# Optimization experiments

Measured on AMD Instinct MI355X. Metric: run time of the kernel, lower is better.

The kernel has to match this reference:

```python
import jax, jax.numpy as jnp
import numpy as np

B, T, C, H = 1, 1024, 2048, 32
N = C // H  # head_dim = 64
EPS_GN = 0.00064


def setup_inputs() -> dict:
    key = jax.random.key(0)
    ks = jax.random.split(key, 40)
    f32 = jnp.float32

    def rn(k, shape, s):
        return jax.random.normal(k, shape, f32) * s

    layer_idx, n_layer = 12, 24
    r01 = layer_idx / (n_layer - 1)
    r1a0 = 1.0 - layer_idx / n_layer
    ddd = (jnp.arange(C, dtype=f32) / C).reshape(1, 1, C)
    decay_speed = -7.0 + 5.0 * (jnp.arange(C, dtype=f32) / (C - 1)) ** (0.85 + r01 ** 0.5)

    inp = dict(
        hidden_states=jax.random.normal(ks[0], (B, T, C), f32),
        Wq=rn(ks[1], (C, C), 0.02), Wk=rn(ks[2], (C, C), 0.02),
        Wv=rn(ks[3], (C, C), 0.02), Wo=rn(ks[4], (C, C), 0.02),
        time_maa_x=1.0 - ddd ** (0.6 * r1a0 ** 0.9),
        time_maa_rg=rn(ks[5], (1, 1, C), 0.01),
        time_maa_wa=rn(ks[6], (1, 1, C), 0.01),
        time_maa_k=rn(ks[7], (1, 1, C), 0.01),
        time_maa_v=rn(ks[8], (1, 1, C), 0.01),
        time_maa_w1=rn(ks[9], (C, 4 * 32), 0.01),
        time_maa_w2=rn(ks[10], (4, 32, C), 0.01),
        time_decay=decay_speed.reshape(1, 1, C) + 0.5,
        time_decay_w1=rn(ks[11], (C, 64), 0.01),
        time_decay_w2=rn(ks[12], (64, C), 0.01),
        time_aaaaa=rn(ks[13], (1, 1, C), 0.01),
        time_aaa_w1=rn(ks[14], (C, 16), 0.01),
        time_aaa_w2=rn(ks[15], (16, C), 0.01),
        time_kkk_w1=rn(ks[16], (C, 16), 0.01),
        time_kkk_w2=rn(ks[17], (16, C), 0.01),
        gate_w1=rn(ks[18], (C, 128), 0.01),
        gate_w2=rn(ks[19], (128, C), 0.01),
        time_misc_a=rn(ks[20], (1, 1, C), 0.01),
        ma_w1=rn(ks[21], (C, 16), 0.01),
        ma_w2=rn(ks[22], (16, C), 0.01),
        time_misc_k=rn(ks[23], (1, 1, C), 0.01),
        mk_w1=rn(ks[24], (C, 16), 0.01),
        mk_w2=rn(ks[25], (16, C), 0.01),
        time_faaaa=rn(ks[26], (1, 1, H, N), 0.01),
        ln_w=1.0 + rn(ks[27], (C,), 0.01),
        ln_b=rn(ks[28], (C,), 0.01),
    )
    return inp


def _wkv7(r, w, k, v, a, b):
    """RWKV7 matrix-state recurrence. Inputs [B,T,C]; per head state [N,N].
    state_t = state * exp(w_t) (per key-col) + (state @ a_t) b_t^T + v_t k_t^T;
    out_t = state_t @ r_t."""
    hs = lambda x: x.reshape(B, T, H, N)
    r, k, v, a, b = map(hs, (r, k, v, a, b))
    dec = jnp.exp(hs(w))  # w <= -0.5, decay in (0,1)

    def step(state, inp):
        r_t, d_t, k_t, v_t, a_t, b_t = inp  # each [B,H,N]
        sa = jnp.einsum('bhij,bhj->bhi', state, a_t)
        state = (state * d_t[:, :, None, :]
                 + sa[..., None] * b_t[:, :, None, :]
                 + v_t[..., None] * k_t[:, :, None, :])
        out = jnp.einsum('bhij,bhj->bhi', state, r_t)
        return state, out

    xs = tuple(jnp.moveaxis(t, 1, 0) for t in (r, dec, k, v, a, b))  # [T,B,H,N]
    state0 = jnp.zeros((B, H, N, N), r.dtype)
    _, out = jax.lax.scan(step, state0, xs)
    return jnp.moveaxis(out, 0, 1).reshape(B, T, C)


def _group_norm(x, w, b):
    xg = x.reshape(B, T, H, N)
    mu = xg.mean(-1, keepdims=True)
    var = xg.var(-1, keepdims=True)
    xn = (xg - mu) * jax.lax.rsqrt(var + EPS_GN)
    return xn.reshape(B, T, C) * w + b


def reference(hidden_states, Wq, Wk, Wv, Wo, time_maa_x, time_maa_rg, time_maa_wa,
              time_maa_k, time_maa_v, time_maa_w1, time_maa_w2, time_decay,
              time_decay_w1, time_decay_w2, time_aaaaa, time_aaa_w1, time_aaa_w2,
              time_kkk_w1, time_kkk_w2, gate_w1, gate_w2, time_misc_a, ma_w1, ma_w2,
              time_misc_k, mk_w1, mk_w2, time_faaaa, ln_w, ln_b):
    x = hidden_states  # T already multiple of 16, so no padding branch
    dxprev = jnp.pad(x, ((0, 0), (1, 0), (0, 0)))[:, :-1] - x  # token shift
    xxx = x + dxprev * time_maa_x
    mix = jnp.tanh(xxx @ time_maa_w1).reshape(B, T, 4, 32)
    mix = jnp.einsum('btfd,fdc->fbtc', mix, time_maa_w2)  # [4,B,T,C]
    mrg, mwa, mk_mix, mv = mix[0], mix[1], mix[2], mix[3]
    xrg = x + dxprev * (time_maa_rg + mrg)
    xwa = x + dxprev * (time_maa_wa + mwa)
    xk = x + dxprev * (time_maa_k + mk_mix)
    xv = x + dxprev * (time_maa_v + mv)

    r = xrg @ Wq
    w = -jax.nn.softplus(-(time_decay + jnp.tanh(xwa @ time_decay_w1) @ time_decay_w2)) - 0.5
    k = xk @ Wk
    v = xv @ Wv
    g = jnp.tanh(xrg @ gate_w1) @ gate_w2

    kk = k + jnp.tanh(xk @ time_kkk_w1) @ time_kkk_w2
    kkh = kk.reshape(B, T, H, N)
    kk = (kkh / jnp.maximum(jnp.linalg.norm(kkh, axis=-1, keepdims=True), 1e-12)).reshape(B, T, C)

    a = jax.nn.sigmoid(time_aaaaa + (xwa @ time_aaa_w1) @ time_aaa_w2)
    ma = jax.nn.sigmoid(time_misc_a + (xwa @ ma_w1) @ ma_w2)
    k = k * ma + k * a * (1.0 - ma)
    mk_g = jax.nn.sigmoid(time_misc_k + (xk @ mk_w1) @ mk_w2)
    k = k * jnp.exp(jnp.minimum(w * mk_g, 0.0))

    y = _wkv7(r, w, k, v, -kk, kk * a)
    y = _group_norm(y, ln_w, ln_b)
    rh, kh, vh = (t.reshape(B, T, H, N) for t in (r, k, v))
    y = y + ((rh * kh * time_faaaa).sum(-1, keepdims=True) * vh).reshape(B, T, C)
    return (y * g) @ Wo
```

## Files before the change

kernel.cpp:

```cpp
#include <hip/hip_runtime.h>


#define T_ 1024
#define C_ 2048
#define H_ 32
#define N_ 64

using half8  = __attribute__((ext_vector_type(8))) _Float16;
using half4  = __attribute__((ext_vector_type(4))) _Float16;
using floatx4 = __attribute__((ext_vector_type(4))) float;

#define DPP_ADD(v, ctrl) \
    ((v) + __int_as_float(__builtin_amdgcn_update_dpp( \
        0, __float_as_int(v), (ctrl), 0xf, 0xf, true)))
#define REDUCE16(v) do { \
    v = DPP_ADD(v, 0xB1); v = DPP_ADD(v, 0x4E); \
    v = DPP_ADD(v, 0x141); v = DPP_ADD(v, 0x140); } while (0)

__device__ __forceinline__ void async_cp16(const void* g, void* l) {
    __builtin_amdgcn_global_load_lds(
        (const __attribute__((address_space(1))) void*)g,
        (__attribute__((address_space(3))) void*)l, 16, 0, 0);
}

__global__ __launch_bounds__(256) void k_tr(
    const float* __restrict__ W0, const float* __restrict__ W1,
    const float* __restrict__ W2, const float* __restrict__ W3,
    _Float16* __restrict__ D0, _Float16* __restrict__ D1,
    _Float16* __restrict__ D2, _Float16* __restrict__ D3)
{
    const int z = blockIdx.z;
    const float* S = (z == 0) ? W0 : (z == 1) ? W1 : (z == 2) ? W2 : W3;
    _Float16* D = (z == 0) ? D0 : (z == 1) ? D1 : (z == 2) ? D2 : D3;
    const int nb = blockIdx.x * 64, kb = blockIdx.y * 64;
    __shared__ __align__(16) float tile[64][65];
    const int tr = threadIdx.x >> 4, tc4 = (threadIdx.x & 15) * 4;
#pragma unroll
    for (int p = 0; p < 4; ++p) {
        int row = p * 16 + tr;
        float4 v = *(const float4*)&S[(size_t)(kb + row) * C_ + nb + tc4];
        tile[row][tc4 + 0] = v.x; tile[row][tc4 + 1] = v.y;
        tile[row][tc4 + 2] = v.z; tile[row][tc4 + 3] = v.w;
    }
    __syncthreads();
#pragma unroll
    for (int p = 0; p < 4; ++p) {
        int n = p * 16 + tr;
        half4 u;
        u[0] = (_Float16)tile[tc4 + 0][n];
        u[1] = (_Float16)tile[tc4 + 1][n];
        u[2] = (_Float16)tile[tc4 + 2][n];
        u[3] = (_Float16)tile[tc4 + 3][n];
        *(half4*)&D[(size_t)(nb + n) * C_ + kb + tc4] = u;
    }
}

__global__ __launch_bounds__(256) void k_trW(
    const float* __restrict__ maa_w1, const float* __restrict__ gate_w1,
    const float* __restrict__ decay_w1, const float* __restrict__ aaa_w1,
    const float* __restrict__ ma_w1, const float* __restrict__ kkk_w1,
    const float* __restrict__ mk_w1,
    _Float16* __restrict__ WTm, _Float16* __restrict__ WTl)
{
    const int z = blockIdx.z;
    const int k = blockIdx.x * 256 + threadIdx.x;
    const int n = blockIdx.y;
    if (z == 0 && n >= 128) return;
    const float* src; int stride, col;
    _Float16* dst;
    if (z == 0) { src = maa_w1; stride = 128; col = n; dst = WTm; }
    else {
        dst = WTl;
        if (n < 128)      { src = gate_w1;  stride = 128; col = n; }
        else if (n < 192) { src = decay_w1; stride = 64;  col = n - 128; }
        else if (n < 208) { src = aaa_w1;   stride = 16;  col = n - 192; }
        else if (n < 224) { src = ma_w1;    stride = 16;  col = n - 208; }
        else if (n < 240) { src = kkk_w1;   stride = 16;  col = n - 224; }
        else              { src = mk_w1;    stride = 16;  col = n - 240; }
    }
    dst[(size_t)n * C_ + k] = (_Float16)src[(size_t)k * stride + col];
}

__global__ __launch_bounds__(256) void k_prep(
    const float* __restrict__ X, const float* __restrict__ maa_x,
    _Float16* __restrict__ xxxH)
{
    const size_t idx = (size_t)blockIdx.x * 256 + threadIdx.x;
    const int c = (int)(idx & (C_ - 1));
    float cur = X[idx];
    float prev = (idx >= C_) ? X[idx - C_] : 0.0f;
    xxxH[idx] = (_Float16)(cur + (prev - cur) * maa_x[c]);
}

__global__ __launch_bounds__(256) void k_lora(
    int which,
    const _Float16* __restrict__ Axxx, const _Float16* __restrict__ Axrg,
    const _Float16* __restrict__ Axwa, const _Float16* __restrict__ Axk,
    const _Float16* __restrict__ WTm, const _Float16* __restrict__ WTl,
    float* __restrict__ m1p, float* __restrict__ l2p)
{
    const int mt = blockIdx.x;
    const int nt = blockIdx.y;
    const int ks = blockIdx.z;
    const _Float16* A; const _Float16* BT; float* O; int ostride;
    if (which == 0) { A = Axxx; BT = WTm; O = m1p; ostride = 128; }
    else {
        BT = WTl; O = l2p; ostride = 256;
        A = (nt < 4) ? Axrg : (nt < 7) ? Axwa : Axk;
    }
    O += (size_t)ks * T_ * ostride;
    const int m0 = mt * 64, n0 = nt * 32, k0 = ks * 512;
    const int tid = threadIdx.x;
    __shared__ __align__(16) _Float16 As[64 * 40];
    __shared__ __align__(16) _Float16 Bs[32 * 40];
    const int lane = tid & 63, wv = tid >> 6;
    const int r16 = lane & 15, q = lane >> 4;

    floatx4 acc[2];
    { floatx4 zv = {0.f, 0.f, 0.f, 0.f}; acc[0] = zv; acc[1] = zv; }

    const int arow = tid >> 2, ac8 = (tid & 3) * 8;
    const _Float16* ag = A + (size_t)(m0 + arow) * C_ + k0 + ac8;
    const _Float16* bg = BT + (size_t)(n0 + (tid >> 2)) * C_ + k0 + ac8;

    for (int kc = 0; kc < 512; kc += 32) {
        half8 av = *(const half8*)(ag + kc);
        half8 bv;
        if (tid < 128) bv = *(const half8*)(bg + kc);
        *(half8*)&As[arow * 40 + ac8] = av;
        if (tid < 128) *(half8*)&Bs[(tid >> 2) * 40 + ac8] = bv;
        __syncthreads();
        half8 af = *(const half8*)&As[(wv * 16 + r16) * 40 + q * 8];
        half8 b0 = *(const half8*)&Bs[(r16) * 40 + q * 8];
        half8 b1 = *(const half8*)&Bs[(16 + r16) * 40 + q * 8];
        acc[0] = __builtin_amdgcn_mfma_f32_16x16x32_f16(af, b0, acc[0], 0, 0, 0);
        acc[1] = __builtin_amdgcn_mfma_f32_16x16x32_f16(af, b1, acc[1], 0, 0, 0);
        __syncthreads();
    }
#pragma unroll
    for (int j = 0; j < 2; ++j)
#pragma unroll
        for (int e = 0; e < 4; ++e) {
            int row = m0 + wv * 16 + q * 4 + e;
            int col = n0 + j * 16 + r16;
            O[(size_t)row * ostride + col] = acc[j][e];
        }
}

__global__ __launch_bounds__(256) void k_xmix(
    const float* __restrict__ X, const float* __restrict__ m1p,
    const float* __restrict__ w2,
    const float* __restrict__ mrg, const float* __restrict__ mwa,
    const float* __restrict__ mk, const float* __restrict__ mv,
    _Float16* __restrict__ xrgH, _Float16* __restrict__ xwaH,
    _Float16* __restrict__ xkH, _Float16* __restrict__ xvH)
{
    const int tid = threadIdx.x;
    const int c = blockIdx.x * 256 + tid;
    const int t0 = blockIdx.y * 16;
    const size_t P = (size_t)T_ * 128;
    __shared__ __align__(16) float m1s[16][128];
#pragma unroll
    for (int p = 0; p < 2; ++p) {
        int id = tid + p * 256;
        int r = id >> 5, c4 = (id & 31) * 4;
        size_t off = (size_t)(t0 + r) * 128 + c4;
        float4 v0 = *(const float4*)&m1p[off];
        float4 v1 = *(const float4*)&m1p[P + off];
        float4 v2 = *(const float4*)&m1p[2 * P + off];
        float4 v3 = *(const float4*)&m1p[3 * P + off];
        float4 v;
        v.x = tanhf(((v0.x + v1.x) + v2.x) + v3.x);
        v.y = tanhf(((v0.y + v1.y) + v2.y) + v3.y);
        v.z = tanhf(((v0.z + v1.z) + v2.z) + v3.z);
        v.w = tanhf(((v0.w + v1.w) + v2.w) + v3.w);
        *(float4*)&m1s[r][c4] = v;
    }
    __syncthreads();
    float a0[16], a1[16], a2[16], a3[16];
#pragma unroll
    for (int t = 0; t < 16; ++t) { a0[t] = 0.f; a1[t] = 0.f; a2[t] = 0.f; a3[t] = 0.f; }
    for (int d = 0; d < 32; ++d) {
        float w0 = w2[(size_t)(0 * 32 + d) * C_ + c];
        float w1 = w2[(size_t)(1 * 32 + d) * C_ + c];
        float w2v = w2[(size_t)(2 * 32 + d) * C_ + c];
        float w3 = w2[(size_t)(3 * 32 + d) * C_ + c];
#pragma unroll
        for (int t = 0; t < 16; ++t) {
            a0[t] = fmaf(m1s[t][d],      w0,  a0[t]);
            a1[t] = fmaf(m1s[t][32 + d], w1,  a1[t]);
            a2[t] = fmaf(m1s[t][64 + d], w2v, a2[t]);
            a3[t] = fmaf(m1s[t][96 + d], w3,  a3[t]);
        }
    }
    float vrg = mrg[c], vwa = mwa[c], vmk = mk[c], vmv = mv[c];
    float prev = (t0 > 0) ? X[(size_t)(t0 - 1) * C_ + c] : 0.0f;
    for (int t = 0; t < 16; ++t) {
        size_t idx = (size_t)(t0 + t) * C_ + c;
        float cur = X[idx];
        float dx = prev - cur;
        xrgH[idx] = (_Float16)(cur + dx * (vrg + a0[t]));
        xwaH[idx] = (_Float16)(cur + dx * (vwa + a1[t]));
        xkH[idx]  = (_Float16)(cur + dx * (vmk + a2[t]));
        xvH[idx]  = (_Float16)(cur + dx * (vmv + a3[t]));
        prev = cur;
    }
}

__global__ __launch_bounds__(256) void k_gemm(
    const _Float16* __restrict__ A0, const _Float16* __restrict__ B0, float* __restrict__ C0,
    const _Float16* __restrict__ A1, const _Float16* __restrict__ B1, float* __restrict__ C1,
    const _Float16* __restrict__ A2, const _Float16* __restrict__ B2, float* __restrict__ C2)
{
    const int z = blockIdx.z;
    const _Float16* A = (z == 0) ? A0 : (z == 1) ? A1 : A2;
    const _Float16* Bt = (z == 0) ? B0 : (z == 1) ? B1 : B2;
    float* C = (z == 0) ? C0 : (z == 1) ? C1 : C2;
    const int mtile = blockIdx.y * 128;
    const int ntile = blockIdx.x * 128;
    const int tid = threadIdx.x;
    __shared__ __align__(16) _Float16 As[2][128 * 32];
    __shared__ __align__(16) _Float16 Bs[2][128 * 32];
    const int lane = tid & 63;
    const int wvid = tid >> 6;
    const int wm = wvid >> 1, wn = wvid & 1;
    const int r16 = lane & 15, q = lane >> 4;

    floatx4 acc[4][4];
#pragma unroll
    for (int i = 0; i < 4; ++i)
#pragma unroll
        for (int j = 0; j < 4; ++j) { floatx4 zv = {0.f, 0.f, 0.f, 0.f}; acc[i][j] = zv; }

    const int srow = tid >> 2, sq = tid & 3;
    const _Float16* agA = A + (size_t)(mtile + srow) * C_ + sq * 8;
    const _Float16* agB = Bt + (size_t)(ntile + srow) * C_ + sq * 8;
    const int ldso = srow * 32 + sq * 8;
    const size_t rowoff = (size_t)64 * C_;

    async_cp16(agA, &As[0][ldso]);
    async_cp16(agA + rowoff, &As[0][ldso + 64 * 32]);
    async_cp16(agB, &Bs[0][ldso]);
    async_cp16(agB + rowoff, &Bs[0][ldso + 64 * 32]);

    for (int kc = 0; kc < C_; kc += 32) {
        const int p = (kc >> 5) & 1;
        __syncthreads();
        if (kc + 32 < C_) {
            async_cp16(agA + kc + 32, &As[p ^ 1][ldso]);
            async_cp16(agA + kc + 32 + rowoff, &As[p ^ 1][ldso + 64 * 32]);
            async_cp16(agB + kc + 32, &Bs[p ^ 1][ldso]);
            async_cp16(agB + kc + 32 + rowoff, &Bs[p ^ 1][ldso + 64 * 32]);
        }
        half8 af[4], bf[4];
#pragma unroll
        for (int i = 0; i < 4; ++i)
            af[i] = *(const half8*)&As[p][(wm * 64 + i * 16 + r16) * 32 + q * 8];
#pragma unroll
        for (int j = 0; j < 4; ++j)
            bf[j] = *(const half8*)&Bs[p][(wn * 64 + j * 16 + r16) * 32 + q * 8];
#pragma unroll
        for (int i = 0; i < 4; ++i)
#pragma unroll
            for (int j = 0; j < 4; ++j)
                acc[i][j] = __builtin_amdgcn_mfma_f32_16x16x32_f16(af[i], bf[j], acc[i][j], 0, 0, 0);
    }
#pragma unroll
    for (int i = 0; i < 4; ++i)
#pragma unroll
        for (int j = 0; j < 4; ++j)
#pragma unroll
            for (int e = 0; e < 4; ++e) {
                int row = mtile + wm * 64 + i * 16 + q * 4 + e;
                int col = ntile + wn * 64 + j * 16 + r16;
                C[(size_t)row * C_ + col] = acc[i][j][e];
            }
}

__global__ __launch_bounds__(256) void k_fuse(
    const float* __restrict__ l2p,
    float* __restrict__ K0,
    const float* __restrict__ decay_w2, const float* __restrict__ aaa_w2,
    const float* __restrict__ ma_w2, const float* __restrict__ kkk_w2,
    const float* __restrict__ mk_w2,
    const float* __restrict__ tdecay, const float* __restrict__ aaaaa,
    const float* __restrict__ misc_a, const float* __restrict__ misc_k,
    float* __restrict__ Dout, float* __restrict__ KKout, float* __restrict__ Bout)
{
    const int tid = threadIdx.x;
    const int c = blockIdx.x * 256 + tid;
    const int t0 = blockIdx.y * 16;
    const size_t P = (size_t)T_ * 256;
    __shared__ __align__(16) float wsS[16][96];
    __shared__ __align__(16) float ksS[16][32];
    for (int id = tid; id < 16 * 24; id += 256) {
        int r = id / 24, c4 = (id % 24) * 4;
        size_t off = (size_t)(t0 + r) * 256 + 128 + c4;
        float4 v0 = *(const float4*)&l2p[off];
        float4 v1 = *(const float4*)&l2p[P + off];
        float4 v2 = *(const float4*)&l2p[2 * P + off];
        float4 v3 = *(const float4*)&l2p[3 * P + off];
        float4 v;
        v.x = ((v0.x + v1.x) + v2.x) + v3.x;
        v.y = ((v0.y + v1.y) + v2.y) + v3.y;
        v.z = ((v0.z + v1.z) + v2.z) + v3.z;
        v.w = ((v0.w + v1.w) + v2.w) + v3.w;
        if (c4 < 64) { v.x = tanhf(v.x); v.y = tanhf(v.y); v.z = tanhf(v.z); v.w = tanhf(v.w); }
        *(float4*)&wsS[r][c4] = v;
    }
    for (int id = tid; id < 16 * 8; id += 256) {
        int r = id / 8, c4 = (id % 8) * 4;
        size_t off = (size_t)(t0 + r) * 256 + 224 + c4;
        float4 v0 = *(const float4*)&l2p[off];
        float4 v1 = *(const float4*)&l2p[P + off];
        float4 v2 = *(const float4*)&l2p[2 * P + off];
        float4 v3 = *(const float4*)&l2p[3 * P + off];
        float4 v;
        v.x = ((v0.x + v1.x) + v2.x) + v3.x;
        v.y = ((v0.y + v1.y) + v2.y) + v3.y;
        v.z = ((v0.z + v1.z) + v2.z) + v3.z;
        v.w = ((v0.w + v1.w) + v2.w) + v3.w;
        if (c4 < 16) { v.x = tanhf(v.x); v.y = tanhf(v.y); v.z = tanhf(v.z); v.w = tanhf(v.w); }
        *(float4*)&ksS[r][c4] = v;
    }
    __syncthreads();
    float accW[16], accA[16], accMA[16], accKK[16], accMK[16];
#pragma unroll
    for (int r = 0; r < 16; ++r) { accW[r] = 0.f; accA[r] = 0.f; accMA[r] = 0.f; accKK[r] = 0.f; accMK[r] = 0.f; }
    for (int j = 0; j < 64; ++j) {
        float w = decay_w2[(size_t)j * C_ + c];
#pragma unroll
        for (int r = 0; r < 16; ++r) accW[r] = fmaf(wsS[r][j], w, accW[r]);
    }
    for (int j = 0; j < 16; ++j) {
        float wa = aaa_w2[(size_t)j * C_ + c];
        float wm = ma_w2[(size_t)j * C_ + c];
        float wk = kkk_w2[(size_t)j * C_ + c];
        float wq = mk_w2[(size_t)j * C_ + c];
#pragma unroll
        for (int r = 0; r < 16; ++r) {
            accA[r]  = fmaf(wsS[r][64 + j], wa, accA[r]);
            accMA[r] = fmaf(wsS[r][80 + j], wm, accMA[r]);
            accKK[r] = fmaf(ksS[r][j],      wk, accKK[r]);
            accMK[r] = fmaf(ksS[r][16 + j], wq, accMK[r]);
        }
    }
    float td = tdecay[c], aa = aaaaa[c], mia = misc_a[c], mik = misc_k[c];
    for (int r = 0; r < 16; ++r) {
        size_t idx = (size_t)(t0 + r) * C_ + c;
        float wraw = td + accW[r];
        float w = -logf(1.0f + __expf(-wraw)) - 0.5f;
        float a  = 1.0f / (1.0f + __expf(-(aa  + accA[r])));
        float mav = 1.0f / (1.0f + __expf(-(mia + accMA[r])));
        float mkv = 1.0f / (1.0f + __expf(-(mik + accMK[r])));
        float k0 = K0[idx];
        float kkun = k0 + accKK[r];
        float ss = kkun * kkun;
        REDUCE16(ss);
        ss += __shfl_xor(ss, 16, 64);
        ss += __shfl_xor(ss, 32, 64);
        float kn = kkun * (1.0f / fmaxf(sqrtf(ss), 1e-12f));
        Dout[idx]  = __expf(w);
        KKout[idx] = kn;
        Bout[idx]  = kn * a;
        K0[idx]    = k0 * (mav + a * (1.0f - mav)) * __expf(fminf(w * mkv, 0.0f));
    }
}

__global__ __launch_bounds__(128) void k_wkv(
    const float* __restrict__ R, const float* __restrict__ DEC,
    const float* __restrict__ K, const float* __restrict__ V,
    const float* __restrict__ KK, const float* __restrict__ Bb,
    float* __restrict__ Y)
{
    const int tid = threadIdx.x;
    const int h = blockIdx.x >> 3;
    const int rg = blockIdx.x & 7;
    const int c0 = h * 64;
    const int wv = tid >> 6, lane = tid & 63;
    const int rowslot = lane >> 4;
    const int lrow = wv * 4 + rowslot;
    const int irow = rg * 8 + lrow;
    const int jg = lane & 15, j4 = jg * 4;

    __shared__ __align__(16) float rS[2][16][64], dS[2][16][64], kS[2][16][64],
                                   aS[2][16][64], bS[2][16][64];
    __shared__ __align__(16) float vS[2][16][8];

    const int s0_step = tid >> 4, s0_q4 = (tid & 15) * 4;
    const int s1_step = (tid + 128) >> 4, s1_q4 = ((tid + 128) & 15) * 4;
    const int v_step = tid >> 1, v_q4 = (tid & 1) * 4;

#define WKV_STAGE(buf, tcb) do {                                              \
    size_t g0 = (size_t)((tcb) + s0_step) * C_ + c0 + s0_q4;                  \
    size_t g1 = (size_t)((tcb) + s1_step) * C_ + c0 + s1_q4;                  \
    async_cp16(&R[g0],   &rS[buf][s0_step][s0_q4]);                           \
    async_cp16(&R[g1],   &rS[buf][s1_step][s1_q4]);                           \
    async_cp16(&DEC[g0], &dS[buf][s0_step][s0_q4]);                           \
    async_cp16(&DEC[g1], &dS[buf][s1_step][s1_q4]);                           \
    async_cp16(&K[g0],   &kS[buf][s0_step][s0_q4]);                           \
    async_cp16(&K[g1],   &kS[buf][s1_step][s1_q4]);                           \
    async_cp16(&KK[g0],  &aS[buf][s0_step][s0_q4]);                           \
    async_cp16(&KK[g1],  &aS[buf][s1_step][s1_q4]);                           \
    async_cp16(&Bb[g0],  &bS[buf][s0_step][s0_q4]);                           \
    async_cp16(&Bb[g1],  &bS[buf][s1_step][s1_q4]);                           \
    if (tid < 32)                                                             \
        async_cp16(&V[(size_t)((tcb) + v_step) * C_ + c0 + rg * 8 + v_q4],    \
                   &vS[buf][v_step][v_q4]);                                   \
} while (0)

    WKV_STAGE(0, 0);

    float4 s = make_float4(0.f, 0.f, 0.f, 0.f);

    for (int tc = 0; tc < T_; tc += 16) {
        const int p = (tc >> 4) & 1;
        __syncthreads();
        if (tc + 16 < T_) WKV_STAGE(p ^ 1, tc + 16);

        float po[16];

        float4 cr = *(float4*)&rS[p][0][j4];
        float4 cd = *(float4*)&dS[p][0][j4];
        float4 ck = *(float4*)&kS[p][0][j4];
        float4 ca = *(float4*)&aS[p][0][j4];
        float4 cb = *(float4*)&bS[p][0][j4];
        float   cv = vS[p][0][lrow];
#pragma unroll
        for (int tt = 0; tt < 16; ++tt) {
            float4 nr, nd, nk, na, nb; float nv = 0.f;
            if (tt < 15) {
                nr = *(float4*)&rS[p][tt + 1][j4];
                nd = *(float4*)&dS[p][tt + 1][j4];
                nk = *(float4*)&kS[p][tt + 1][j4];
                na = *(float4*)&aS[p][tt + 1][j4];
                nb = *(float4*)&bS[p][tt + 1][j4];
                nv = vS[p][tt + 1][lrow];
            }
            float d01 = fmaf(s.y, ca.y, s.x * ca.x);
            float d23 = fmaf(s.w, ca.w, s.z * ca.z);
            float sa = -(d01 + d23);
            REDUCE16(sa);
            s.x = fmaf(s.x, cd.x, fmaf(sa, cb.x, cv * ck.x));
            s.y = fmaf(s.y, cd.y, fmaf(sa, cb.y, cv * ck.y));
            s.z = fmaf(s.z, cd.z, fmaf(sa, cb.z, cv * ck.z));
            s.w = fmaf(s.w, cd.w, fmaf(sa, cb.w, cv * ck.w));
            po[tt] = fmaf(s.w, cr.w, fmaf(s.z, cr.z, fmaf(s.y, cr.y, s.x * cr.x)));
            cr = nr; cd = nd; ck = nk; ca = na; cb = nb; cv = nv;
        }
#pragma unroll
        for (int tt = 0; tt < 16; ++tt) REDUCE16(po[tt]);
        if (jg == 0) {
#pragma unroll
            for (int tt = 0; tt < 16; ++tt)
                Y[(size_t)(tc + tt) * C_ + c0 + irow] = po[tt];
        }
    }
#undef WKV_STAGE
}

__global__ __launch_bounds__(256) void k_gn(
    const float* __restrict__ Y, const float* __restrict__ R, const float* __restrict__ K,
    const float* __restrict__ V, const float* __restrict__ l2p,
    const float* __restrict__ gw2,
    const float* __restrict__ faaaa, const float* __restrict__ lnw,
    const float* __restrict__ lnb, _Float16* __restrict__ YG)
{
    const int tid = threadIdx.x;
    const int c = blockIdx.x * 256 + tid;
    const int t0 = blockIdx.y * 16;
    const size_t P = (size_t)T_ * 256;
    __shared__ __align__(16) float gs[16][128];
    for (int id = tid; id < 16 * 128; id += 256) {
        int r = id >> 7, cc = id & 127;
        size_t off = (size_t)(t0 + r) * 256 + cc;
        float v = ((l2p[off] + l2p[P + off]) + l2p[2 * P + off]) + l2p[3 * P + off];
        gs[r][cc] = tanhf(v);
    }
    __syncthreads();
    float gacc[16];
#pragma unroll
    for (int r = 0; r < 16; ++r) gacc[r] = 0.f;
    for (int j = 0; j < 128; ++j) {
        float w = gw2[(size_t)j * C_ + c];
#pragma unroll
        for (int r = 0; r < 16; ++r) gacc[r] = fmaf(gs[r][j], w, gacc[r]);
    }
    float fa = faaaa[c], lw = lnw[c], lb = lnb[c];
    for (int r = 0; r < 16; ++r) {
        const size_t idx = (size_t)(t0 + r) * C_ + c;
        float y = Y[idx];
        float s1 = y, s2 = y * y;
#pragma unroll
        for (int off = 1; off < 64; off <<= 1) {
            s1 += __shfl_xor(s1, off, 64);
            s2 += __shfl_xor(s2, off, 64);
        }
        float mu = s1 * (1.0f / 64.0f);
        float var = s2 * (1.0f / 64.0f) - mu * mu;
        float gn = (y - mu) * rsqrtf(var + 0.00064f) * lw + lb;
        float p = R[idx] * K[idx] * fa;
#pragma unroll
        for (int off = 1; off < 64; off <<= 1) p += __shfl_xor(p, off, 64);
        float y2 = gn + p * V[idx];
        YG[idx] = (_Float16)(y2 * gacc[r]);
    }
}

extern "C" void kernel_launch(void* const* d_in, const int* in_sizes, int n_in,
                              void* d_out, int out_size, void* d_ws, size_t ws_size,
                              hipStream_t stream)
{
    (void)in_sizes; (void)n_in; (void)out_size; (void)ws_size;
    const float* hidden   = (const float*)d_in[0];
    const float* Wq       = (const float*)d_in[1];
    const float* Wk       = (const float*)d_in[2];
    const float* Wv       = (const float*)d_in[3];
    const float* Wo       = (const float*)d_in[4];
    const float* maa_x    = (const float*)d_in[5];
    const float* maa_rg   = (const float*)d_in[6];
    const float* maa_wa   = (const float*)d_in[7];
    const float* maa_k    = (const float*)d_in[8];
    const float* maa_v    = (const float*)d_in[9];
    const float* maa_w1   = (const float*)d_in[10];
    const float* maa_w2   = (const float*)d_in[11];
    const float* tdecay   = (const float*)d_in[12];
    const float* decay_w1 = (const float*)d_in[13];
    const float* decay_w2 = (const float*)d_in[14];
    const float* aaaaa    = (const float*)d_in[15];
    const float* aaa_w1   = (const float*)d_in[16];
    const float* aaa_w2   = (const float*)d_in[17];
    const float* kkk_w1   = (const float*)d_in[18];
    const float* kkk_w2   = (const float*)d_in[19];
    const float* gate_w1  = (const float*)d_in[20];
    const float* gate_w2  = (const float*)d_in[21];
    const float* misc_a   = (const float*)d_in[22];
    const float* ma_w1    = (const float*)d_in[23];
    const float* ma_w2    = (const float*)d_in[24];
    const float* misc_k   = (const float*)d_in[25];
    const float* mk_w1    = (const float*)d_in[26];
    const float* mk_w2    = (const float*)d_in[27];
    const float* faaaa    = (const float*)d_in[28];
    const float* lnw      = (const float*)d_in[29];
    const float* lnb      = (const float*)d_in[30];

    float* ws = (float*)d_ws;
    const size_t TC = (size_t)T_ * C_;
    float* S0 = ws + 0 * TC;
    float* S2 = ws + 2 * TC;
    float* S3 = ws + 3 * TC;
    float* S4 = ws + 4 * TC;
    float* S5 = ws + 5 * TC;
    float* S6 = ws + 6 * TC;
    float* S7 = ws + 7 * TC;
    float* m1p = ws + 8 * TC;
    float* l2p = m1p + (size_t)4 * T_ * 128;
    _Float16* WTq = (_Float16*)(l2p + (size_t)4 * T_ * 256);
    _Float16* WTk = WTq + (size_t)C_ * C_;
    _Float16* WTv = WTk + (size_t)C_ * C_;
    _Float16* WTo = WTv + (size_t)C_ * C_;
    _Float16* WTm = WTo + (size_t)C_ * C_;
    _Float16* WTl = WTm + (size_t)128 * C_;
    _Float16* xxxH = WTl + (size_t)256 * C_;
    _Float16* xrgH = xxxH + TC;
    _Float16* xwaH = xrgH + TC;
    _Float16* xkH  = xwaH + TC;
    _Float16* xvH  = xkH + TC;
    _Float16* ygH  = xxxH;
    float* out = (float*)d_out;

    k_tr<<<dim3(32, 32, 4), 256, 0, stream>>>(Wq, Wk, Wv, Wo, WTq, WTk, WTv, WTo);
    k_trW<<<dim3(8, 256, 2), 256, 0, stream>>>(maa_w1, gate_w1, decay_w1,
        aaa_w1, ma_w1, kkk_w1, mk_w1, WTm, WTl);
    k_prep<<<dim3((int)(TC / 256)), 256, 0, stream>>>(hidden, maa_x, xxxH);
    k_lora<<<dim3(16, 4, 4), 256, 0, stream>>>(0, xxxH, xxxH, xxxH, xxxH,
        WTm, WTl, m1p, l2p);
    k_xmix<<<dim3(8, 64), 256, 0, stream>>>(hidden, m1p, maa_w2,
        maa_rg, maa_wa, maa_k, maa_v, xrgH, xwaH, xkH, xvH);
    k_lora<<<dim3(16, 8, 4), 256, 0, stream>>>(1, xxxH, xrgH, xwaH, xkH,
        WTm, WTl, m1p, l2p);
    k_gemm<<<dim3(16, 8, 3), 256, 0, stream>>>(
        xrgH, WTq, S4,  xkH, WTk, S6,  xvH, WTv, S7);
    k_fuse<<<dim3(8, 64), 256, 0, stream>>>(l2p, S6, decay_w2, aaa_w2, ma_w2,
        kkk_w2, mk_w2, tdecay, aaaaa, misc_a, misc_k, S5, S3, S2);
    k_wkv<<<dim3(256), 128, 0, stream>>>(S4, S5, S6, S7, S3, S2, S0);
    k_gn<<<dim3(8, 64), 256, 0, stream>>>(S0, S4, S6, S7, l2p, gate_w2,
        faaaa, lnw, lnb, ygH);
    k_gemm<<<dim3(16, 8, 1), 256, 0, stream>>>(
        ygH, WTo, out,  ygH, WTo, out,  ygH, WTo, out);
}
```

Measured before the change: 572.8 us.

## Parallelize WKV7 recurrence over time chunks with a state-transition scan

```diff
diff --git a/kernel.cpp b/kernel.cpp
--- a/kernel.cpp
+++ b/kernel.cpp
@@ -367,96 +367,221 @@
     }
 }
 
-__global__ __launch_bounds__(128) void k_wkv(
+__global__ __launch_bounds__(1024) void k_wkv_p1(
+    const float* __restrict__ DEC, const float* __restrict__ K,
+    const float* __restrict__ V, const float* __restrict__ KK,
+    const float* __restrict__ Bb,
+    float* __restrict__ Send, float* __restrict__ Pend)
+{
+    const int tid = threadIdx.x;
+    const int g = blockIdx.x;
+    const int h = blockIdx.y;
+    const bool isP = blockIdx.z != 0;
+    const int c0 = h * 64;
+    const int wv = tid >> 6, lane = tid & 63;
+    const int row = wv * 4 + (lane >> 4);
+    const int jg = lane & 15, j4 = jg * 4;
+
+    __shared__ __align__(16) float dS[2][16][64], aS[2][16][64], bS[2][16][64],
+                                   kS[2][16][64], vS[2][16][64];
+
+    const int pos = tid & 255, grp = tid >> 8;
+    const int pst = pos >> 4, pq4 = (pos & 15) * 4;
+
+#define P1_STAGE(buf, tcb) do {                                               \
+    size_t gg = (size_t)((tcb) + pst) * C_ + c0 + pq4;                        \
+    if (grp == 0)      async_cp16(&DEC[gg], &dS[buf][pst][pq4]);              \
+    else if (grp == 2) async_cp16(&KK[gg],  &aS[buf][pst][pq4]);              \
+    else if (grp == 3) async_cp16(&Bb[gg],  &bS[buf][pst][pq4]);              \
+    if (!isP) {                                                               \
+        if (grp == 1)      async_cp16(&K[gg], &kS[buf][pst][pq4]);            \
+        else if (grp == 0) async_cp16(&V[gg], &vS[buf][pst][pq4]);            \
+    }                                                                         \
+} while (0)
+
+    float4 s;
+    if (isP) {
+        s.x = (j4 + 0 == row) ? 1.f : 0.f;
+        s.y = (j4 + 1 == row) ? 1.f : 0.f;
+        s.z = (j4 + 2 == row) ? 1.f : 0.f;
+        s.w = (j4 + 3 == row) ? 1.f : 0.f;
+    } else {
+        s = make_float4(0.f, 0.f, 0.f, 0.f);
+    }
+
+    const int t0 = g * 128;
+    P1_STAGE(0, t0);
+
+    if (isP) {
+        for (int tc = 0; tc < 128; tc += 16) {
+            const int p = (tc >> 4) & 1;
+            __syncthreads();
+            if (tc + 16 < 128) P1_STAGE(p ^ 1, t0 + tc + 16);
+#pragma unroll
+            for (int tt = 0; tt < 16; ++tt) {
+                float4 cd = *(float4*)&dS[p][tt][j4];
+                float4 ca = *(float4*)&aS[p][tt][j4];
+                float4 cb = *(float4*)&bS[p][tt][j4];
+                float d01 = fmaf(s.y, ca.y, s.x * ca.x);
+                float d23 = fmaf(s.w, ca.w, s.z * ca.z);
+                float sa = -(d01 + d23);
+                REDUCE16(sa);
+                s.x = fmaf(s.x, cd.x, sa * cb.x);
+                s.y = fmaf(s.y, cd.y, sa * cb.y);
+                s.z = fmaf(s.z, cd.z, sa * cb.z);
+                s.w = fmaf(s.w, cd.w, sa * cb.w);
+            }
+        }
+        *(float4*)&Pend[(size_t)((h * 7 + g) * 64 + row) * 64 + j4] = s;
+    } else {
+        for (int tc = 0; tc < 128; tc += 16) {
+            const int p = (tc >> 4) & 1;
+            __syncthreads();
+            if (tc + 16 < 128) P1_STAGE(p ^ 1, t0 + tc + 16);
+#pragma unroll
+            for (int tt = 0; tt < 16; ++tt) {
+                float4 cd = *(float4*)&dS[p][tt][j4];
+                float4 ca = *(float4*)&aS[p][tt][j4];
+                float4 cb = *(float4*)&bS[p][tt][j4];
+                float4 ck = *(float4*)&kS[p][tt][j4];
+                float  cv = vS[p][tt][row];
+                float d01 = fmaf(s.y, ca.y, s.x * ca.x);
+                float d23 = fmaf(s.w, ca.w, s.z * ca.z);
+                float sa = -(d01 + d23);
+                REDUCE16(sa);
+                s.x = fmaf(s.x, cd.x, fmaf(sa, cb.x, cv * ck.x));
+                s.y = fmaf(s.y, cd.y, fmaf(sa, cb.y, cv * ck.y));
+                s.z = fmaf(s.z, cd.z, fmaf(sa, cb.z, cv * ck.z));
+                s.w = fmaf(s.w, cd.w, fmaf(sa, cb.w, cv * ck.w));
+            }
+        }
+        *(float4*)&Send[(size_t)((h * 7 + g) * 64 + row) * 64 + j4] = s;
+    }
+#undef P1_STAGE
+}
+
+__global__ __launch_bounds__(256) void k_wkv_comb(
+    const float* __restrict__ Send, const float* __restrict__ Pend,
+    float* __restrict__ Sin)
+{
+    const int h = blockIdx.x;
+    const int tid = threadIdx.x;
+    const int i = tid >> 2;
+    const int jq = (tid & 3) * 16;
+    __shared__ float Sc[64][65];
+    __shared__ __align__(16) float Pl[64][64];
+
+    float4 z4 = make_float4(0.f, 0.f, 0.f, 0.f);
+#pragma unroll
+    for (int c = 0; c < 16; c += 4)
+        *(float4*)&Sin[(size_t)(h * 8) * 4096 + (size_t)i * 64 + jq + c] = z4;
+#pragma unroll
+    for (int c = 0; c < 16; ++c) Sc[i][jq + c] = 0.f;
+    __syncthreads();
+
+    for (int g = 1; g < 8; ++g) {
+        const float* Pg = &Pend[(size_t)(h * 7 + g - 1) * 4096];
+        for (int idx = tid * 4; idx < 4096; idx += 1024) {
+            float4 v = *(const float4*)&Pg[idx];
+            *(float4*)&Pl[idx >> 6][idx & 63] = v;
+        }
+        __syncthreads();
+        float acc[16];
+        const float* Sg = &Send[(size_t)(h * 7 + g - 1) * 4096 + (size_t)i * 64 + jq];
+#pragma unroll
+        for (int c = 0; c < 16; c += 4) {
+            float4 v = *(const float4*)&Sg[c];
+            acc[c] = v.x; acc[c + 1] = v.y; acc[c + 2] = v.z; acc[c + 3] = v.w;
+        }
+        for (int k = 0; k < 64; ++k) {
+            float sik = Sc[i][k];
+#pragma unroll
+            for (int c = 0; c < 16; ++c) acc[c] = fmaf(sik, Pl[k][jq + c], acc[c]);
+        }
+        __syncthreads();
+        float* So = &Sin[(size_t)(h * 8 + g) * 4096 + (size_t)i * 64 + jq];
+#pragma unroll
+        for (int c = 0; c < 16; ++c) Sc[i][jq + c] = acc[c];
+#pragma unroll
+        for (int c = 0; c < 16; c += 4) {
+            float4 v = make_float4(acc[c], acc[c + 1], acc[c + 2], acc[c + 3]);
+            *(float4*)&So[c] = v;
+        }
+        __syncthreads();
+    }
+}
+
+__global__ __launch_bounds__(1024) void k_wkv_p2(
     const float* __restrict__ R, const float* __restrict__ DEC,
     const float* __restrict__ K, const float* __restrict__ V,
     const float* __restrict__ KK, const float* __restrict__ Bb,
-    float* __restrict__ Y)
+    const float* __restrict__ Sin, float* __restrict__ Y)
 {
     const int tid = threadIdx.x;
-    const int h = blockIdx.x >> 3;
-    const int rg = blockIdx.x & 7;
+    const int g = blockIdx.x;
+    const int h = blockIdx.y;
     const int c0 = h * 64;
     const int wv = tid >> 6, lane = tid & 63;
-    const int rowslot = lane >> 4;
-    const int lrow = wv * 4 + rowslot;
-    const int irow = rg * 8 + lrow;
+    const int row = wv * 4 + (lane >> 4);
     const int jg = lane & 15, j4 = jg * 4;
 
     __shared__ __align__(16) float rS[2][16][64], dS[2][16][64], kS[2][16][64],
-                                   aS[2][16][64], bS[2][16][64];
-    __shared__ __align__(16) float vS[2][16][8];
-
-    const int s0_step = tid >> 4, s0_q4 = (tid & 15) * 4;
-    const int s1_step = (tid + 128) >> 4, s1_q4 = ((tid + 128) & 15) * 4;
-    const int v_step = tid >> 1, v_q4 = (tid & 1) * 4;
-
-#define WKV_STAGE(buf, tcb) do {                                              \
-    size_t g0 = (size_t)((tcb) + s0_step) * C_ + c0 + s0_q4;                  \
-    size_t g1 = (size_t)((tcb) + s1_step) * C_ + c0 + s1_q4;                  \
-    async_cp16(&R[g0],   &rS[buf][s0_step][s0_q4]);                           \
-    async_cp16(&R[g1],   &rS[buf][s1_step][s1_q4]);                           \
-    async_cp16(&DEC[g0], &dS[buf][s0_step][s0_q4]);                           \
-    async_cp16(&DEC[g1], &dS[buf][s1_step][s1_q4]);                           \
-    async_cp16(&K[g0],   &kS[buf][s0_step][s0_q4]);                           \
-    async_cp16(&K[g1],   &kS[buf][s1_step][s1_q4]);                           \
-    async_cp16(&KK[g0],  &aS[buf][s0_step][s0_q4]);                           \
-    async_cp16(&KK[g1],  &aS[buf][s1_step][s1_q4]);                           \
-    async_cp16(&Bb[g0],  &bS[buf][s0_step][s0_q4]);                           \
-    async_cp16(&Bb[g1],  &bS[buf][s1_step][s1_q4]);                           \
-    if (tid < 32)                                                             \
-        async_cp16(&V[(size_t)((tcb) + v_step) * C_ + c0 + rg * 8 + v_q4],    \
-                   &vS[buf][v_step][v_q4]);                                   \
+                                   aS[2][16][64], bS[2][16][64], vS[2][16][64];
+
+    const int pos = tid & 255, grp = tid >> 8;
+    const int pst = pos >> 4, pq4 = (pos & 15) * 4;
+
+#define P2_STAGE(buf, tcb) do {                                               \
+    size_t gg = (size_t)((tcb) + pst) * C_ + c0 + pq4;                        \
+    if (grp == 0)      { async_cp16(&R[gg], &rS[buf][pst][pq4]);              \
+                         async_cp16(&K[gg], &kS[buf][pst][pq4]); }            \
+    else if (grp == 1) { async_cp16(&DEC[gg], &dS[buf][pst][pq4]);            \
+                         async_cp16(&V[gg],   &vS[buf][pst][pq4]); }          \
+    else if (grp == 2) async_cp16(&KK[gg], &aS[buf][pst][pq4]);               \
+    else               async_cp16(&Bb[gg], &bS[buf][pst][pq4]);               \
 } while (0)
 
-    WKV_STAGE(0, 0);
-
-    float4 s = make_float4(0.f, 0.f, 0.f, 0.f);
-
-    for (int tc = 0; tc < T_; tc += 16) {
+    float4 s = *(const float4*)&Sin[(size_t)((h * 8 + g) * 64 + row) * 64 + j4];
+
+    const int t0 = g * 128;
+    P2_STAGE(0, t0);
+
+    for (int tc = 0; tc < 128; tc += 16) {
         const int p = (tc >> 4) & 1;
         __syncthreads();
-        if (tc + 16 < T_) WKV_STAGE(p ^ 1, tc + 16);
-
-        float po[16];
-
-        float4 cr = *(float4*)&rS[p][0][j4];
-        float4 cd = *(float4*)&dS[p][0][j4];
-        float4 ck = *(float4*)&kS[p][0][j4];
-        float4 ca = *(float4*)&aS[p][0][j4];
-        float4 cb = *(float4*)&bS[p][0][j4];
-        float   cv = vS[p][0][lrow];
-#pragma unroll
-        for (int tt = 0; tt < 16; ++tt) {
-            float4 nr, nd, nk, na, nb; float nv = 0.f;
-            if (tt < 15) {
-                nr = *(float4*)&rS[p][tt + 1][j4];
-                nd = *(float4*)&dS[p][tt + 1][j4];
-                nk = *(float4*)&kS[p][tt + 1][j4];
-                na = *(float4*)&aS[p][tt + 1][j4];
-                nb = *(float4*)&bS[p][tt + 1][j4];
-                nv = vS[p][tt + 1][lrow];
+        if (tc + 16 < 128) P2_STAGE(p ^ 1, t0 + tc + 16);
+#pragma unroll
+        for (int hh = 0; hh < 2; ++hh) {
+            float po[8];
+#pragma unroll
+            for (int q = 0; q < 8; ++q) {
+                const int tt = hh * 8 + q;
+                float4 cr = *(float4*)&rS[p][tt][j4];
+                float4 cd = *(float4*)&dS[p][tt][j4];
+                float4 ck = *(float4*)&kS[p][tt][j4];
+                float4 ca = *(float4*)&aS[p][tt][j4];
+                float4 cb = *(float4*)&bS[p][tt][j4];
+                float  cv = vS[p][tt][row];
+                float d01 = fmaf(s.y, ca.y, s.x * ca.x);
+                float d23 = fmaf(s.w, ca.w, s.z * ca.z);
+                float sa = -(d01 + d23);
+                REDUCE16(sa);
+                s.x = fmaf(s.x, cd.x, fmaf(sa, cb.x, cv * ck.x));
+                s.y = fmaf(s.y, cd.y, fmaf(sa, cb.y, cv * ck.y));
+                s.z = fmaf(s.z, cd.z, fmaf(sa, cb.z, cv * ck.z));
+                s.w = fmaf(s.w, cd.w, fmaf(sa, cb.w, cv * ck.w));
+                po[q] = fmaf(s.w, cr.w, fmaf(s.z, cr.z, fmaf(s.y, cr.y, s.x * cr.x)));
             }
-            float d01 = fmaf(s.y, ca.y, s.x * ca.x);
-            float d23 = fmaf(s.w, ca.w, s.z * ca.z);
-            float sa = -(d01 + d23);
-            REDUCE16(sa);
-            s.x = fmaf(s.x, cd.x, fmaf(sa, cb.x, cv * ck.x));
-            s.y = fmaf(s.y, cd.y, fmaf(sa, cb.y, cv * ck.y));
-            s.z = fmaf(s.z, cd.z, fmaf(sa, cb.z, cv * ck.z));
-            s.w = fmaf(s.w, cd.w, fmaf(sa, cb.w, cv * ck.w));
-            po[tt] = fmaf(s.w, cr.w, fmaf(s.z, cr.z, fmaf(s.y, cr.y, s.x * cr.x)));
-            cr = nr; cd = nd; ck = nk; ca = na; cb = nb; cv = nv;
-        }
-#pragma unroll
-        for (int tt = 0; tt < 16; ++tt) REDUCE16(po[tt]);
-        if (jg == 0) {
-#pragma unroll
-            for (int tt = 0; tt < 16; ++tt)
-                Y[(size_t)(tc + tt) * C_ + c0 + irow] = po[tt];
-        }
-    }
-#undef WKV_STAGE
+#pragma unroll
+            for (int q = 0; q < 8; ++q) REDUCE16(po[q]);
+            if (jg == 0) {
+#pragma unroll
+                for (int q = 0; q < 8; ++q)
+                    Y[(size_t)(t0 + tc + hh * 8 + q) * C_ + c0 + row] = po[q];
+            }
+        }
+    }
+#undef P2_STAGE
 }
 
 __global__ __launch_bounds__(256) void k_gn(
@@ -547,6 +672,8 @@
     float* ws = (float*)d_ws;
     const size_t TC = (size_t)T_ * C_;
     float* S0 = ws + 0 * TC;
+    float* Send = ws + 1 * TC;
+    float* Pend = Send + (size_t)32 * 7 * 64 * 64;
     float* S2 = ws + 2 * TC;
     float* S3 = ws + 3 * TC;
     float* S4 = ws + 4 * TC;
@@ -567,6 +694,7 @@
     _Float16* xkH  = xwaH + TC;
     _Float16* xvH  = xkH + TC;
     _Float16* ygH  = xxxH;
+    float* Sin = (float*)xrgH;
     float* out = (float*)d_out;
 
     k_tr<<<dim3(32, 32, 4), 256, 0, stream>>>(Wq, Wk, Wv, Wo, WTq, WTk, WTv, WTo);
@@ -583,7 +711,9 @@
         xrgH, WTq, S4,  xkH, WTk, S6,  xvH, WTv, S7);
     k_fuse<<<dim3(8, 64), 256, 0, stream>>>(l2p, S6, decay_w2, aaa_w2, ma_w2,
         kkk_w2, mk_w2, tdecay, aaaaa, misc_a, misc_k, S5, S3, S2);
-    k_wkv<<<dim3(256), 128, 0, stream>>>(S4, S5, S6, S7, S3, S2, S0);
+    k_wkv_p1<<<dim3(7, 32, 2), 1024, 0, stream>>>(S5, S6, S7, S3, S2, Send, Pend);
+    k_wkv_comb<<<dim3(32), 256, 0, stream>>>(Send, Pend, Sin);
+    k_wkv_p2<<<dim3(8, 32), 1024, 0, stream>>>(S4, S5, S6, S7, S3, S2, Sin, S0);
     k_gn<<<dim3(8, 64), 256, 0, stream>>>(S0, S4, S6, S7, l2p, gate_w2,
         faaaa, lnw, lnb, ygH);
     k_gemm<<<dim3(16, 8, 1), 256, 0, stream>>>(
```

Result: faster. 558.1 us (-2.6%).
